# Optimization experiments

Measured on AMD Instinct MI355X. Metric: run time of the kernel, lower is better.

Reference implementation:

```python
import jax, jax.numpy as jnp
import numpy as np

INT8_MAX = 127.0

def _quant_ste(x, axis):
    """Dynamic symmetric int8 fake-quant along `axis` (per-channel scales).
    Returns dequantized values; math matches int8 dot * scales (AQT-style)."""
    amax = jnp.max(jnp.abs(x), axis=axis, keepdims=True)
    scale = jnp.maximum(amax, 1e-6) / INT8_MAX
    q = jnp.clip(jnp.round(x / scale), -INT8_MAX, INT8_MAX)
    return q * scale

def setup_inputs() -> dict:
    key = jax.random.key(0)
    k1, k2 = jax.random.split(key)
    inputs = jax.random.normal(k1, (4, 2048, 4096), dtype=jnp.float32)
    kernel = jax.random.normal(k2, (4096, 4096), dtype=jnp.float32) * 0.02
    return {"inputs": inputs, "kernel": kernel}

def reference(inputs, kernel):
    # eqn: '...y,yz->...z' with quantized dot_general:
    # per-row (last-axis) dynamic int8 quant of activations,
    # per-output-column int8 quant of kernel, int8 matmul, dequant by scales.
    xq = _quant_ste(inputs, axis=-1)   # [B, S, D]
    kq = _quant_ste(kernel, axis=0)    # [D, F]
    return jnp.einsum('bsd,df->bsf', xq, kq)  # [B, S, F]
```

## Files before the change

kernel.cpp:

```cpp
#include <hip/hip_runtime.h>


#define M_DIM 8192
#define K_DIM 4096
#define N_DIM 4096

typedef int v4i __attribute__((ext_vector_type(4)));
typedef __attribute__((address_space(3))) void lds_void_t;
typedef const __attribute__((address_space(1))) void g_void_t;

__global__ __launch_bounds__(1024) void fused_prep(
    const float* __restrict__ X, const float* __restrict__ W,
    signed char* __restrict__ At, float* __restrict__ sx,
    float* __restrict__ part) {
  const int t = threadIdx.x;

  if (blockIdx.x < 32) {
    const int slab = blockIdx.x;
    const float4* p = (const float4*)W + (size_t)slab * 128 * 1024 + t;
    float4 a = {0.f, 0.f, 0.f, 0.f};
#pragma unroll 8
    for (int i = 0; i < 128; ++i) {
      float4 u = p[(size_t)i * 1024];
      a.x = fmaxf(a.x, fabsf(u.x));
      a.y = fmaxf(a.y, fabsf(u.y));
      a.z = fmaxf(a.z, fabsf(u.z));
      a.w = fmaxf(a.w, fabsf(u.w));
    }
    ((float4*)part)[(size_t)slab * 1024 + t] = a;
    return;
  }

  const int tile = blockIdx.x - 32;
  const int row = t >> 6;
  const int j = t & 63;
  const float4* xr = (const float4*)X + ((size_t)tile * 16 + row) * 1024;

  float4 v[4][4];
  float am = 0.f;
#pragma unroll
  for (int u = 0; u < 4; ++u)
#pragma unroll
    for (int c = 0; c < 4; ++c) {
      v[u][c] = xr[(u * 64 + j) * 4 + c];
      am = fmaxf(am, fmaxf(fmaxf(fabsf(v[u][c].x), fabsf(v[u][c].y)),
                           fmaxf(fabsf(v[u][c].z), fabsf(v[u][c].w))));
    }
#pragma unroll
  for (int off = 32; off > 0; off >>= 1)
    am = fmaxf(am, __shfl_down(am, off));
  am = __shfl(am, 0);
  const float scale = fmaxf(am, 1e-6f) / 127.0f;
  if (j == 0) sx[tile * 16 + row] = scale;
  const float inv = 1.0f / scale;

  signed char* tb = At + (size_t)tile * 65536 + row * 16;
#pragma unroll
  for (int u = 0; u < 4; ++u) {
    unsigned int d[4];
#pragma unroll
    for (int c = 0; c < 4; ++c) {
      int q0 = (int)fminf(fmaxf(rintf(v[u][c].x * inv), -127.f), 127.f);
      int q1 = (int)fminf(fmaxf(rintf(v[u][c].y * inv), -127.f), 127.f);
      int q2 = (int)fminf(fmaxf(rintf(v[u][c].z * inv), -127.f), 127.f);
      int q3 = (int)fminf(fmaxf(rintf(v[u][c].w * inv), -127.f), 127.f);
      d[c] = (q0 & 255) | ((q1 & 255) << 8) | ((q2 & 255) << 16) | (q3 << 24);
    }
    v4i w = {(int)d[0], (int)d[1], (int)d[2], (int)d[3]};
    *(v4i*)(tb + (u * 64 + j) * 256) = w;
  }
}

__global__ void wk_quant(const float* __restrict__ W,
                         const float* __restrict__ part,
                         signed char* __restrict__ Bt,
                         float* __restrict__ sk) {
  const int bx = blockIdx.x;
  const int f0 = (bx & 63) * 64;
  const int d0 = (bx >> 6) * 64;
  const int t = threadIdx.x;
  const int fl4 = t & 15;
  const int dl0 = t >> 4;
  __shared__ __align__(16) signed char tile[64 * 80];
  __shared__ float sl_inv[64];

  float4 wv[4];
#pragma unroll
  for (int c = 0; c < 4; ++c) {
    const int dl = c * 16 + dl0;
    wv[c] = ((const float4*)W)[(size_t)(d0 + dl) * 1024 + (f0 >> 2) + fl4];
  }
  if (t < 64) {
    const int f = f0 + t;
    float m = 0.f;
#pragma unroll
    for (int s = 0; s < 32; ++s) m = fmaxf(m, part[(size_t)s * 4096 + f]);
    const float scale = fmaxf(m, 1e-6f) / 127.0f;
    if (bx < 64) sk[f] = scale;
    sl_inv[t] = 1.0f / scale;
  }
  __syncthreads();
  const float4 inv4 = *(const float4*)&sl_inv[fl4 * 4];
#pragma unroll
  for (int c = 0; c < 4; ++c) {
    const int dl = c * 16 + dl0;
    tile[(fl4 * 4 + 0) * 80 + dl] =
        (signed char)(int)fminf(fmaxf(rintf(wv[c].x * inv4.x), -127.f), 127.f);
    tile[(fl4 * 4 + 1) * 80 + dl] =
        (signed char)(int)fminf(fmaxf(rintf(wv[c].y * inv4.y), -127.f), 127.f);
    tile[(fl4 * 4 + 2) * 80 + dl] =
        (signed char)(int)fminf(fmaxf(rintf(wv[c].z * inv4.z), -127.f), 127.f);
    tile[(fl4 * 4 + 3) * 80 + dl] =
        (signed char)(int)fminf(fmaxf(rintf(wv[c].w * inv4.w), -127.f), 127.f);
  }
  __syncthreads();
  const int frow = t >> 2;
  const int ksl = t & 3;
  v4i w = *(const v4i*)&tile[frow * 80 + ksl * 16];
  const int f = f0 + frow;
  signed char* dst = Bt + (size_t)(f >> 4) * 65536 + ((d0 >> 4) + ksl) * 256 +
                     (f & 15) * 16;
  *(v4i*)dst = w;
}

__global__ __launch_bounds__(256, 2) void gemm_i8(
    const signed char* __restrict__ At, const signed char* __restrict__ Bt,
    const float* __restrict__ sx, const float* __restrict__ sk,
    float* __restrict__ C) {
  const int n0 = blockIdx.x * 128;
  const int m0 = blockIdx.y * 128;
  const int t = threadIdx.x;
  const int lane = t & 63;
  const int wave = t >> 6;
  const int wm = (wave >> 1) * 64;
  const int wn = (wave & 1) * 64;
  const int lrow = lane & 15;
  const int lq = lane >> 4;

  __shared__ __align__(16) signed char lds[32768];
  signed char* lA = lds;
  signed char* lB = lds + 16384;

  v4i acc[4][4];
#pragma unroll
  for (int i = 0; i < 4; ++i)
#pragma unroll
    for (int j = 0; j < 4; ++j) acc[i][j] = (v4i){0, 0, 0, 0};

  const signed char* Abase = At + (size_t)(m0 >> 4) * 65536;
  const signed char* Bbase = Bt + (size_t)(n0 >> 4) * 65536;

  const int la = ((wave >> 1) * 4) * 2048 + lane * 16;
  const int lb = ((wave & 1) * 4) * 2048 + lane * 16;

  for (int kb = 0; kb < K_DIM; kb += 128) {
    const int kofs = kb * 16;
#pragma unroll
    for (int j = 0; j < 4; ++j) {
      const int c = j * 256 + t;
      const int mt_i = c >> 7;
      const int inner = c & 127;
      __builtin_amdgcn_global_load_lds(
          (g_void_t*)(Abase + (size_t)mt_i * 65536 + kofs + inner * 16),
          (lds_void_t*)(lA + c * 16), 16, 0, 0);
      __builtin_amdgcn_global_load_lds(
          (g_void_t*)(Bbase + (size_t)mt_i * 65536 + kofs + inner * 16),
          (lds_void_t*)(lB + c * 16), 16, 0, 0);
    }
    __syncthreads();
#pragma unroll
    for (int s = 0; s < 2; ++s) {
      v4i af[4], bf[4];
#pragma unroll
      for (int i = 0; i < 4; ++i) af[i] = *(const v4i*)(lA + la + i * 2048 + s * 1024);
#pragma unroll
      for (int i = 0; i < 4; ++i) bf[i] = *(const v4i*)(lB + lb + i * 2048 + s * 1024);
#pragma unroll
      for (int mi = 0; mi < 4; ++mi)
#pragma unroll
        for (int ni = 0; ni < 4; ++ni)
          acc[mi][ni] =
              __builtin_amdgcn_mfma_i32_16x16x64_i8(af[mi], bf[ni], acc[mi][ni], 0, 0, 0);
    }
    __syncthreads();
  }

#pragma unroll
  for (int mi = 0; mi < 4; ++mi) {
#pragma unroll
    for (int ni = 0; ni < 4; ++ni) {
      const int gn = n0 + wn + ni * 16 + lrow;
      const float skv = sk[gn];
#pragma unroll
      for (int r = 0; r < 4; ++r) {
        const int gm = m0 + wm + mi * 16 + lq * 4 + r;
        C[(size_t)gm * N_DIM + gn] = (float)acc[mi][ni][r] * sx[gm] * skv;
      }
    }
  }
}

extern "C" void kernel_launch(void* const* d_in, const int* in_sizes, int n_in,
                              void* d_out, int out_size, void* d_ws, size_t ws_size,
                              hipStream_t stream) {
  const float* X = (const float*)d_in[0];
  const float* W = (const float*)d_in[1];
  float* out = (float*)d_out;
  char* ws = (char*)d_ws;

  signed char* At = (signed char*)ws;
  signed char* Bt = (signed char*)(ws + 33554432);
  float* sx = (float*)(ws + 50331648);
  float* sk = (float*)(ws + 50364416);
  float* part = (float*)(ws + 50380800);

  fused_prep<<<544, 1024, 0, stream>>>(X, W, At, sx, part);
  wk_quant<<<4096, 256, 0, stream>>>(W, part, Bt, sk);
  gemm_i8<<<dim3(N_DIM / 128, M_DIM / 128), 256, 0, stream>>>(At, Bt, sx, sk, out);
}
```

Baseline: 426.5 us.

## Enlarge GEMM M-tile to 256 and split weight amax reduction across more blocks

The int8 GEMM block tile grows from 128x128 to 256x128, so each wave computes a 128x64 sub-tile with 32 accumulators. This raises arithmetic intensity per LDS load and halves the reloads of B tiles. The cost is higher register pressure, 48KB of LDS, and half as many blocks, which may lower occupancy under launch_bounds(256,2). Separately, the weight column amax pass is spread over 256 blocks with an in-block LDS reduction instead of 32 blocks, giving more parallelism in the prep kernel.

```diff
diff --git a/kernel.cpp b/kernel.cpp
--- a/kernel.cpp
+++ b/kernel.cpp
@@ -14,24 +14,41 @@
     signed char* __restrict__ At, float* __restrict__ sx,
     float* __restrict__ part) {
   const int t = threadIdx.x;
-
-  if (blockIdx.x < 32) {
-    const int slab = blockIdx.x;
-    const float4* p = (const float4*)W + (size_t)slab * 128 * 1024 + t;
+  __shared__ float4 wred[1024];
+
+  if (blockIdx.x < 256) {
+    const int slab = blockIdx.x >> 3;
+    const int cg = blockIdx.x & 7;
+    const int c4 = cg * 128 + (t & 127);
+    const int r0 = t >> 7;
+    const float4* p = (const float4*)W + ((size_t)slab * 128 + r0) * 1024 + c4;
     float4 a = {0.f, 0.f, 0.f, 0.f};
-#pragma unroll 8
-    for (int i = 0; i < 128; ++i) {
-      float4 u = p[(size_t)i * 1024];
+#pragma unroll
+    for (int i = 0; i < 16; ++i) {
+      float4 u = p[(size_t)i * 8192];
       a.x = fmaxf(a.x, fabsf(u.x));
       a.y = fmaxf(a.y, fabsf(u.y));
       a.z = fmaxf(a.z, fabsf(u.z));
       a.w = fmaxf(a.w, fabsf(u.w));
     }
-    ((float4*)part)[(size_t)slab * 1024 + t] = a;
+    wred[t] = a;
+    __syncthreads();
+    if (t < 128) {
+      float4 m = wred[t];
+#pragma unroll
+      for (int j = 1; j < 8; ++j) {
+        float4 u = wred[t + j * 128];
+        m.x = fmaxf(m.x, u.x);
+        m.y = fmaxf(m.y, u.y);
+        m.z = fmaxf(m.z, u.z);
+        m.w = fmaxf(m.w, u.w);
+      }
+      ((float4*)part)[(size_t)slab * 1024 + c4] = m;
+    }
     return;
   }
 
-  const int tile = blockIdx.x - 32;
+  const int tile = blockIdx.x - 256;
   const int row = t >> 6;
   const int j = t & 63;
   const float4* xr = (const float4*)X + ((size_t)tile * 16 + row) * 1024;
@@ -128,55 +145,57 @@
     const float* __restrict__ sx, const float* __restrict__ sk,
     float* __restrict__ C) {
   const int n0 = blockIdx.x * 128;
-  const int m0 = blockIdx.y * 128;
+  const int m0 = blockIdx.y * 256;
   const int t = threadIdx.x;
   const int lane = t & 63;
   const int wave = t >> 6;
-  const int wm = (wave >> 1) * 64;
+  const int wm = (wave >> 1) * 128;
   const int wn = (wave & 1) * 64;
   const int lrow = lane & 15;
   const int lq = lane >> 4;
 
-  __shared__ __align__(16) signed char lds[32768];
+  __shared__ __align__(16) signed char lds[49152];
   signed char* lA = lds;
-  signed char* lB = lds + 16384;
-
-  v4i acc[4][4];
-#pragma unroll
-  for (int i = 0; i < 4; ++i)
+  signed char* lB = lds + 32768;
+
+  v4i acc[8][4];
+#pragma unroll
+  for (int i = 0; i < 8; ++i)
 #pragma unroll
     for (int j = 0; j < 4; ++j) acc[i][j] = (v4i){0, 0, 0, 0};
 
   const signed char* Abase = At + (size_t)(m0 >> 4) * 65536;
   const signed char* Bbase = Bt + (size_t)(n0 >> 4) * 65536;
 
-  const int la = ((wave >> 1) * 4) * 2048 + lane * 16;
-  const int lb = ((wave & 1) * 4) * 2048 + lane * 16;
+  const int la = (wm >> 4) * 2048 + lane * 16;
+  const int lb = (wn >> 4) * 2048 + lane * 16;
 
   for (int kb = 0; kb < K_DIM; kb += 128) {
     const int kofs = kb * 16;
 #pragma unroll
+    for (int j = 0; j < 8; ++j) {
+      const int c = j * 256 + t;
+      __builtin_amdgcn_global_load_lds(
+          (g_void_t*)(Abase + (size_t)(c >> 7) * 65536 + kofs + (c & 127) * 16),
+          (lds_void_t*)(lA + c * 16), 16, 0, 0);
+    }
+#pragma unroll
     for (int j = 0; j < 4; ++j) {
       const int c = j * 256 + t;
-      const int mt_i = c >> 7;
-      const int inner = c & 127;
       __builtin_amdgcn_global_load_lds(
-          (g_void_t*)(Abase + (size_t)mt_i * 65536 + kofs + inner * 16),
-          (lds_void_t*)(lA + c * 16), 16, 0, 0);
-      __builtin_amdgcn_global_load_lds(
-          (g_void_t*)(Bbase + (size_t)mt_i * 65536 + kofs + inner * 16),
+          (g_void_t*)(Bbase + (size_t)(c >> 7) * 65536 + kofs + (c & 127) * 16),
           (lds_void_t*)(lB + c * 16), 16, 0, 0);
     }
     __syncthreads();
 #pragma unroll
     for (int s = 0; s < 2; ++s) {
-      v4i af[4], bf[4];
-#pragma unroll
-      for (int i = 0; i < 4; ++i) af[i] = *(const v4i*)(lA + la + i * 2048 + s * 1024);
+      v4i af[8], bf[4];
+#pragma unroll
+      for (int i = 0; i < 8; ++i) af[i] = *(const v4i*)(lA + la + i * 2048 + s * 1024);
 #pragma unroll
       for (int i = 0; i < 4; ++i) bf[i] = *(const v4i*)(lB + lb + i * 2048 + s * 1024);
 #pragma unroll
-      for (int mi = 0; mi < 4; ++mi)
+      for (int mi = 0; mi < 8; ++mi)
 #pragma unroll
         for (int ni = 0; ni < 4; ++ni)
           acc[mi][ni] =
@@ -186,7 +205,7 @@
   }
 
 #pragma unroll
-  for (int mi = 0; mi < 4; ++mi) {
+  for (int mi = 0; mi < 8; ++mi) {
 #pragma unroll
     for (int ni = 0; ni < 4; ++ni) {
       const int gn = n0 + wn + ni * 16 + lrow;
@@ -214,7 +233,7 @@
   float* sk = (float*)(ws + 50364416);
   float* part = (float*)(ws + 50380800);
 
-  fused_prep<<<544, 1024, 0, stream>>>(X, W, At, sx, part);
+  fused_prep<<<768, 1024, 0, stream>>>(X, W, At, sx, part);
   wk_quant<<<4096, 256, 0, stream>>>(W, part, Bt, sk);
-  gemm_i8<<<dim3(N_DIM / 128, M_DIM / 128), 256, 0, stream>>>(At, Bt, sx, sk, out);
-}
+  gemm_i8<<<dim3(N_DIM / 128, M_DIM / 256), 256, 0, stream>>>(At, Bt, sx, sk, out);
+}
```

After: 410.8 us. -3.7%, faster.
